# Optimization experiments

Hardware: AMD Instinct MI355X
Metric: run time of the kernel (lower is better)

The kernel has to match this reference:

```python
import jax, jax.numpy as jnp
import numpy as np

N = 50000      # nodes
E = 800000     # edges (before self-loops)
D_IN = 256     # input feature dim
H = 4          # attention heads
C = 32         # per-head channels
HID = H * C    # 128, concat output dim
BN_EPS = 1e-5


def setup_inputs() -> dict:
    key = jax.random.key(0)
    ks = jax.random.split(key, 24)
    inp = {}
    inp["x"] = jax.random.normal(ks[0], (N, D_IN), jnp.float32)
    inp["edge_index"] = jax.random.randint(ks[1], (2, E), 0, N, jnp.int32)
    # layer 1 GATConv params
    inp["W1"] = jax.random.normal(ks[2], (D_IN, HID), jnp.float32) * (2.0 / (D_IN + HID)) ** 0.5
    inp["att_src1"] = jax.random.normal(ks[3], (H, C), jnp.float32) * 0.1
    inp["att_dst1"] = jax.random.normal(ks[4], (H, C), jnp.float32) * 0.1
    inp["bias1"] = jnp.zeros((HID,), jnp.float32)
    # layer 1 BatchNorm (eval mode)
    inp["gamma1"] = 1.0 + 0.1 * jax.random.normal(ks[5], (HID,), jnp.float32)
    inp["beta1"] = 0.1 * jax.random.normal(ks[6], (HID,), jnp.float32)
    inp["mean1"] = 0.1 * jax.random.normal(ks[7], (HID,), jnp.float32)
    inp["var1"] = 0.5 + jax.random.uniform(ks[8], (HID,), jnp.float32)
    # layer 2 GATConv params
    inp["W2"] = jax.random.normal(ks[9], (HID, HID), jnp.float32) * (2.0 / (HID + HID)) ** 0.5
    inp["att_src2"] = jax.random.normal(ks[10], (H, C), jnp.float32) * 0.1
    inp["att_dst2"] = jax.random.normal(ks[11], (H, C), jnp.float32) * 0.1
    inp["bias2"] = jnp.zeros((HID,), jnp.float32)
    # layer 2 BatchNorm (eval mode)
    inp["gamma2"] = 1.0 + 0.1 * jax.random.normal(ks[12], (HID,), jnp.float32)
    inp["beta2"] = 0.1 * jax.random.normal(ks[13], (HID,), jnp.float32)
    inp["mean2"] = 0.1 * jax.random.normal(ks[14], (HID,), jnp.float32)
    inp["var2"] = 0.5 + jax.random.uniform(ks[15], (HID,), jnp.float32)
    return inp


def _gat_layer(x, src, dst, W, att_src, att_dst, bias):
    # x: [N, D]; src/dst: [Etot] with self-loops already appended
    h = (x @ W).reshape(N, H, C)                       # [N, H, C]
    a_s = jnp.einsum("nhc,hc->nh", h, att_src)         # [N, H]
    a_d = jnp.einsum("nhc,hc->nh", h, att_dst)         # [N, H]
    e = jax.nn.leaky_relu(a_s[src] + a_d[dst], 0.2)    # [Etot, H]
    # edge softmax over incoming edges of each destination node
    m = jax.ops.segment_max(e, dst, num_segments=N)    # [N, H]
    ex = jnp.exp(e - m[dst])                           # [Etot, H]
    den = jax.ops.segment_sum(ex, dst, num_segments=N) # [N, H]
    alpha = ex / (den[dst] + 1e-16)                    # [Etot, H]
    out = jax.ops.segment_sum(h[src] * alpha[:, :, None], dst, num_segments=N)
    return out.reshape(N, HID) + bias                  # concat heads + bias


def _bn_eval(x, gamma, beta, mean, var):
    return (x - mean) * (gamma * jax.lax.rsqrt(var + BN_EPS)) + beta


def reference(x, edge_index, W1, att_src1, att_dst1, bias1, gamma1, beta1, mean1, var1,
              W2, att_src2, att_dst2, bias2, gamma2, beta2, mean2, var2):
    loop = jnp.arange(N, dtype=edge_index.dtype)
    src = jnp.concatenate([edge_index[0], loop])  # PyG GATConv adds self-loops
    dst = jnp.concatenate([edge_index[1], loop])
    h = _gat_layer(x, src, dst, W1, att_src1, att_dst1, bias1)
    h = jax.nn.relu(_bn_eval(h, gamma1, beta1, mean1, var1))  # dropout = identity (eval)
    h = _gat_layer(h, src, dst, W2, att_src2, att_dst2, bias2)
    h = jax.nn.relu(_bn_eval(h, gamma2, beta2, mean2, var2))
    return h
```

## Files before the change

kernel.cpp:

```cpp
#include <hip/hip_runtime.h>
#include <math.h>

#define N_NODES 50000
#define EDGES   800000
#define ETOT    (EDGES + N_NODES)
#define HID     128
#define NH      4

typedef __attribute__((ext_vector_type(8))) short short8;
typedef __attribute__((ext_vector_type(4))) float floatx4;

__device__ inline unsigned short f2bf(float f) {
    unsigned int u = __float_as_uint(f);
    u = u + 0x7FFFu + ((u >> 16) & 1u);
    return (unsigned short)(u >> 16);
}

#define NB 391
#define BCAP 2688
#define CHUNK 4096
#define BIN_BLOCKS ((ETOT + CHUNK - 1) / CHUNK)
#define G1A 391

__device__ __forceinline__ void bin_scatter_body(int* histL, int bid,
                                                 const int* __restrict__ ei,
                                                 int* __restrict__ cursor,
                                                 int* __restrict__ binned) {
    int t = threadIdx.x;
    for (int b = t; b < NB; b += 256) histL[b] = 0;
    __syncthreads();
    int base = bid * CHUNK;
#pragma unroll
    for (int j = 0; j < 16; j++) {
        int e = base + j * 256 + t;
        if (e < ETOT) {
            int d = (e < EDGES) ? ei[EDGES + e] : (e - EDGES);
            atomicAdd(&histL[d >> 7], 1);
        }
    }
    __syncthreads();
    for (int b = t; b < NB; b += 256) {
        int c = histL[b];
        histL[b] = c ? (b * BCAP + atomicAdd(&cursor[b], c)) : 0;
    }
    __syncthreads();
#pragma unroll
    for (int j = 0; j < 16; j++) {
        int e = base + j * 256 + t;
        if (e < ETOT) {
            int s, d;
            if (e < EDGES) { s = ei[e]; d = ei[EDGES + e]; }
            else           { s = d = e - EDGES; }
            int bb = d >> 7;
            int pos = atomicAdd(&histL[bb], 1);
            if (pos < (bb + 1) * BCAP)
                binned[pos] = (s << 7) | (d & 127);
        }
    }
}

__device__ __forceinline__ void bin_finalize_body(int* histN, int* excl, int b,
                                                  const int* __restrict__ binned,
                                                  const int* __restrict__ cursor,
                                                  int* __restrict__ starts,
                                                  int* __restrict__ degs,
                                                  int* __restrict__ csr) {
    int t = threadIdx.x;
    int n0 = b << 7;
    int S = b * BCAP;
    int cnt = cursor[b];
    if (cnt > BCAP) cnt = BCAP;
    if (t < 128) histN[t] = 0;
    __syncthreads();
    for (int j = t; j < cnt; j += 256)
        atomicAdd(&histN[binned[S + j] & 127], 1);
    __syncthreads();
    int v = (t < 128) ? histN[t] : 0;
    if (t < 128) excl[t] = v;
    __syncthreads();
    for (int off = 1; off < 128; off <<= 1) {
        int x = 0, add = 0;
        if (t < 128) { x = excl[t]; if (t >= off) add = excl[t - off]; }
        __syncthreads();
        if (t < 128) excl[t] = x + add;
        __syncthreads();
    }
    if (t < 128) {
        int ex = excl[t] - v;
        int n = n0 + t;
        if (n < N_NODES) { starts[n] = S + ex; degs[n] = v; }
        histN[t] = ex;
    }
    __syncthreads();
    for (int j = t; j < cnt; j += 256) {
        int e = binned[S + j];
        int pos = atomicAdd(&histN[e & 127], 1);
        csr[S + pos] = e >> 7;
    }
}

__global__ void wtrans_coef_kernel(const float* __restrict__ W1, const float* __restrict__ W2,
                                   unsigned short* __restrict__ Wt1, unsigned short* __restrict__ Wt2,
                                   const float* __restrict__ b1, const float* __restrict__ g1,
                                   const float* __restrict__ be1, const float* __restrict__ mn1,
                                   const float* __restrict__ vr1,
                                   const float* __restrict__ b2, const float* __restrict__ g2,
                                   const float* __restrict__ be2, const float* __restrict__ mn2,
                                   const float* __restrict__ vr2, float* __restrict__ coef,
                                   int* __restrict__ cursor) {
    int i = blockIdx.x * 256 + threadIdx.x;
    if (i < NB) cursor[i] = 0;
    if (i < 256 * 128) { int k = i >> 7, n = i & 127; Wt1[n * 256 + k] = f2bf(W1[i]); }
    if (i < 128 * 128) { int k = i >> 7, n = i & 127; Wt2[n * 128 + k] = f2bf(W2[i]); }
    if (blockIdx.x == 0) {
        int t = threadIdx.x;
        if (t < 128) {
            float sc = g1[t] * rsqrtf(vr1[t] + 1e-5f);
            coef[t]       = sc;
            coef[128 + t] = be1[t] + (b1[t] - mn1[t]) * sc;
        } else {
            int c = t - 128;
            float sc = g2[c] * rsqrtf(vr2[c] + 1e-5f);
            coef[256 + c] = sc;
            coef[384 + c] = be2[c] + (b2[c] - mn2[c]) * sc;
        }
    }
}

#define GR   64
#define KC   64
#define PADK 88
#define PADH 136

union Smem {
    struct { unsigned short Xs[GR][PADK]; unsigned short Ws[HID][PADK]; } s;
    unsigned short Hs[GR][PADH];
};

template<bool XBF16>
__device__ __forceinline__ void gemm_att_body(Smem& sm, int bid,
                                              const void* __restrict__ Xv,
                                              const unsigned short* __restrict__ Wt,
                                              const float* __restrict__ att_src,
                                              const float* __restrict__ att_dst,
                                              unsigned short* __restrict__ Hout,
                                              float* __restrict__ aS,
                                              float* __restrict__ aD, int K) {
    int t = threadIdx.x, lane = t & 63, w = t >> 6;
    int quad = lane >> 4, nl = lane & 15;
    int rowBase = bid * GR;

    floatx4 acc[8];
    floatx4 zero = {0.f, 0.f, 0.f, 0.f};
#pragma unroll
    for (int b = 0; b < 8; b++) acc[b] = zero;

    const float*          Xf = (const float*)Xv;
    const unsigned short* Xb = (const unsigned short*)Xv;

    for (int k0 = 0; k0 < K; k0 += KC) {
#pragma unroll
        for (int it = 0; it < 2; it++) {
            int s5 = t + it * 256;
            int row = s5 >> 3, kg = s5 & 7;
            int gr = rowBase + row;
            unsigned short tmp[8];
            if (XBF16) {
                uint4 v = make_uint4(0, 0, 0, 0);
                if (gr < N_NODES) v = *(const uint4*)&Xb[(unsigned)(gr * K + k0 + kg * 8)];
                *(uint4*)tmp = v;
            } else {
                float4 v0 = make_float4(0, 0, 0, 0), v1 = v0;
                if (gr < N_NODES) {
                    const float* p = &Xf[(unsigned)(gr * K + k0 + kg * 8)];
                    v0 = *(const float4*)p;
                    v1 = *(const float4*)(p + 4);
                }
                tmp[0] = f2bf(v0.x); tmp[1] = f2bf(v0.y); tmp[2] = f2bf(v0.z); tmp[3] = f2bf(v0.w);
                tmp[4] = f2bf(v1.x); tmp[5] = f2bf(v1.y); tmp[6] = f2bf(v1.z); tmp[7] = f2bf(v1.w);
            }
            *(uint4*)&sm.s.Xs[row][kg * 8] = *(uint4*)tmp;
        }
#pragma unroll
        for (int it = 0; it < 4; it++) {
            int s5 = t + it * 256;
            int n = s5 >> 3, kg = s5 & 7;
            *(uint4*)&sm.s.Ws[n][kg * 8] = *(const uint4*)&Wt[(unsigned)(n * K + k0 + kg * 8)];
        }
        __syncthreads();
#pragma unroll
        for (int ks = 0; ks < 2; ks++) {
            int kb = ks * 32 + quad * 8;
            short8 a0 = *(const short8*)&sm.s.Xs[w * 16 + nl][kb];
#pragma unroll
            for (int ct = 0; ct < 8; ct++) {
                short8 b = *(const short8*)&sm.s.Ws[ct * 16 + nl][kb];
                acc[ct] = __builtin_amdgcn_mfma_f32_16x16x32_bf16(a0, b, acc[ct], 0, 0, 0);
            }
        }
        __syncthreads();
    }

#pragma unroll
    for (int ct = 0; ct < 8; ct++)
#pragma unroll
        for (int r = 0; r < 4; r++)
            sm.Hs[w * 16 + quad * 4 + r][ct * 16 + nl] = f2bf(acc[ct][r]);

    float asv[8], adv[8];
    {
        const float* ap = &att_src[nl * 8];
        const float* dp = &att_dst[nl * 8];
        *(float4*)&asv[0] = *(const float4*)ap;  *(float4*)&asv[4] = *(const float4*)(ap + 4);
        *(float4*)&adv[0] = *(const float4*)dp;  *(float4*)&adv[4] = *(const float4*)(dp + 4);
    }
    int hd = nl >> 2;
#pragma unroll
    for (int it = 0; it < 4; it++) {
        int rl = w * 16 + it * 4 + quad;
        int grow = rowBase + rl;
        uint4 v = *(const uint4*)&sm.Hs[rl][nl * 8];
        float f[8];
        f[0] = __uint_as_float(v.x << 16); f[1] = __uint_as_float(v.x & 0xffff0000u);
        f[2] = __uint_as_float(v.y << 16); f[3] = __uint_as_float(v.y & 0xffff0000u);
        f[4] = __uint_as_float(v.z << 16); f[5] = __uint_as_float(v.z & 0xffff0000u);
        f[6] = __uint_as_float(v.w << 16); f[7] = __uint_as_float(v.w & 0xffff0000u);
        float ds = 0.f, dd = 0.f;
#pragma unroll
        for (int j = 0; j < 8; j++) {
            ds = fmaf(f[j], asv[j], ds);
            dd = fmaf(f[j], adv[j], dd);
        }
        ds += __shfl_xor(ds, 1); ds += __shfl_xor(ds, 2);
        dd += __shfl_xor(dd, 1); dd += __shfl_xor(dd, 2);
        if (grow < N_NODES) {
            *(uint4*)&Hout[(unsigned)(grow * HID + nl * 8)] = v;
            if ((nl & 3) == 0) { aS[grow * 4 + hd] = ds; aD[grow * 4 + hd] = dd; }
        }
    }
}

__global__ __launch_bounds__(256) void fused_scatter_gemm1a(
        const int* __restrict__ ei, int* __restrict__ cursor, int* __restrict__ binned,
        const float* __restrict__ x, const unsigned short* __restrict__ Wt1,
        const float* __restrict__ att_src, const float* __restrict__ att_dst,
        unsigned short* __restrict__ Hout, float* __restrict__ aS, float* __restrict__ aD) {
    __shared__ Smem sm;
    __shared__ int histL[NB];
    if (blockIdx.x < BIN_BLOCKS) {
        bin_scatter_body(histL, blockIdx.x, ei, cursor, binned);
    } else {
        gemm_att_body<false>(sm, blockIdx.x - BIN_BLOCKS, x, Wt1, att_src, att_dst,
                             Hout, aS, aD, 256);
    }
}

__global__ __launch_bounds__(256) void fused_finalize_gemm1b(
        const int* __restrict__ binned, const int* __restrict__ cursor,
        int* __restrict__ starts, int* __restrict__ degs, int* __restrict__ csr,
        const float* __restrict__ x, const unsigned short* __restrict__ Wt1,
        const float* __restrict__ att_src, const float* __restrict__ att_dst,
        unsigned short* __restrict__ Hout, float* __restrict__ aS, float* __restrict__ aD) {
    __shared__ Smem sm;
    __shared__ int histN[128];
    __shared__ int excl[128];
    if (blockIdx.x < NB) {
        bin_finalize_body(histN, excl, blockIdx.x, binned, cursor, starts, degs, csr);
    } else {
        gemm_att_body<false>(sm, blockIdx.x, x, Wt1, att_src, att_dst,
                             Hout, aS, aD, 256);
    }
}

template<bool XBF16>
__global__ __launch_bounds__(256) void gemm_att_kernel(const void* __restrict__ Xv,
                                                       const unsigned short* __restrict__ Wt,
                                                       const float* __restrict__ att_src,
                                                       const float* __restrict__ att_dst,
                                                       unsigned short* __restrict__ Hout,
                                                       float* __restrict__ aS,
                                                       float* __restrict__ aD, int K) {
    __shared__ Smem sm;
    gemm_att_body<XBF16>(sm, blockIdx.x, Xv, Wt, att_src, att_dst, Hout, aS, aD, K);
}

#define ECAP 64

__device__ __forceinline__ void prefetchR(uint4 (&buf)[4], int sregr, const char* hbase,
                                          int sBase, int l16b) {
#pragma unroll
    for (int u = 0; u < 4; u++) {
        int se = __builtin_amdgcn_ds_bpermute(sBase | (u << 2), sregr);
        buf[u] = *(const uint4*)(hbase + (((long)se) << 8) + l16b);
    }
}

__device__ __forceinline__ void consumeR(const uint4 (&buf)[4], float xrr, int aBase,
                                         float (&acc)[8]) {
#pragma unroll
    for (int u = 0; u < 4; u++) {
        float au = __uint_as_float((unsigned)__builtin_amdgcn_ds_bpermute(
                        aBase | (u << 2), (int)__float_as_uint(xrr)));
        uint4 v = buf[u];
        acc[0] = fmaf(__uint_as_float(v.x << 16),         au, acc[0]);
        acc[1] = fmaf(__uint_as_float(v.x & 0xffff0000u), au, acc[1]);
        acc[2] = fmaf(__uint_as_float(v.y << 16),         au, acc[2]);
        acc[3] = fmaf(__uint_as_float(v.y & 0xffff0000u), au, acc[3]);
        acc[4] = fmaf(__uint_as_float(v.z << 16),         au, acc[4]);
        acc[5] = fmaf(__uint_as_float(v.z & 0xffff0000u), au, acc[5]);
        acc[6] = fmaf(__uint_as_float(v.w << 16),         au, acc[6]);
        acc[7] = fmaf(__uint_as_float(v.w & 0xffff0000u), au, acc[7]);
    }
}

template<bool OUTBF16>
__global__ __launch_bounds__(256) void gather_kernel(const unsigned short* __restrict__ hfeat,
                                                     const float* __restrict__ a_s,
                                                     const float* __restrict__ a_d,
                                                     const int* __restrict__ starts,
                                                     const int* __restrict__ degs,
                                                     const int* __restrict__ csr,
                                                     const float* __restrict__ coefA,
                                                     const float* __restrict__ coefB,
                                                     void* __restrict__ outv) {
    int t = threadIdx.x, lane = t & 63, ws = t >> 6;
    int h = lane >> 4, l16 = lane & 15;
    int n = blockIdx.x * 4 + ws;
    int start = starts[n];
    int deg = degs[n];
    float adh = a_d[(unsigned)(n * 4 + h)];
    const char* hbase = (const char*)hfeat;
    int sBase = lane & 48;
    int aBase = ((lane & 12) << 4) | sBase;
    int l16b = l16 << 4;

    int sreg[4];
#pragma unroll
    for (int it = 0; it < 4; it++) {
        int j = l16 + it * 16;
        sreg[it] = (j < deg) ? csr[start + j] : 0;
    }
    float e[4];
#pragma unroll
    for (int it = 0; it < 4; it++) {
        int j = l16 + it * 16;
        e[it] = -1e30f;
        if (j < deg) {
            float as = a_s[(unsigned)(sreg[it] * 4 + h)];
            float v = as + adh;
            e[it] = v > 0.f ? v : 0.2f * v;
        }
    }

    int cap = deg < ECAP ? deg : ECAP;
    uint4 vA[4], vB[4];
    prefetchR(vA, sreg[0], hbase, sBase, l16b);
    if (cap > 16) prefetchR(vB, sreg[1], hbase, sBase, l16b);

    float m = fmaxf(fmaxf(e[0], e[1]), fmaxf(e[2], e[3]));
    for (int j = ECAP + l16; j < deg; j += 16) {
        int s = csr[start + j];
        float as = a_s[(unsigned)(s * 4 + h)];
        float v = as + adh; v = v > 0.f ? v : 0.2f * v;
        m = fmaxf(m, v);
    }
#pragma unroll
    for (int off = 1; off < 16; off <<= 1) m = fmaxf(m, __shfl_xor(m, off));

    float x[4];
    float d = 0.f;
#pragma unroll
    for (int it = 0; it < 4; it++) { x[it] = __expf(e[it] - m); d += x[it]; }
    for (int j = ECAP + l16; j < deg; j += 16) {
        int s = csr[start + j];
        float as = a_s[(unsigned)(s * 4 + h)];
        float v = as + adh; v = v > 0.f ? v : 0.2f * v;
        d += __expf(v - m);
    }
#pragma unroll
    for (int off = 1; off < 16; off <<= 1) d += __shfl_xor(d, off);
    float rd = 1.0f / (d + 1e-16f);
    float xr[4];
#pragma unroll
    for (int it = 0; it < 4; it++) xr[it] = x[it] * rd;

    float acc[8];
#pragma unroll
    for (int j = 0; j < 8; j++) acc[j] = 0.f;
    consumeR(vA, xr[0], aBase, acc);
    if (cap > 16) {
        if (cap > 32) prefetchR(vA, sreg[2], hbase, sBase, l16b);
        consumeR(vB, xr[1], aBase, acc);
        if (cap > 32) {
            if (cap > 48) prefetchR(vB, sreg[3], hbase, sBase, l16b);
            consumeR(vA, xr[2], aBase, acc);
            if (cap > 48) consumeR(vB, xr[3], aBase, acc);
        }
    }
    if (deg > ECAP) {
        int hh = l16 >> 2;
        int gB = (lane & 12) << 4;
        float mB  = __uint_as_float((unsigned)__builtin_amdgcn_ds_bpermute(gB, (int)__float_as_uint(m)));
        float rdB = __uint_as_float((unsigned)__builtin_amdgcn_ds_bpermute(gB, (int)__float_as_uint(rd)));
        float adhB = a_d[(unsigned)(n * 4 + hh)];
        for (int j = ECAP; j < deg; j++) {
            int s = csr[start + j];
            float asv = a_s[(unsigned)(s * 4 + hh)];
            float v2 = asv + adhB; v2 = v2 > 0.f ? v2 : 0.2f * v2;
            float al = __expf(v2 - mB) * rdB;
            uint4 v = *(const uint4*)(hbase + (((long)s) << 8) + l16b);
            acc[0] = fmaf(__uint_as_float(v.x << 16),         al, acc[0]);
            acc[1] = fmaf(__uint_as_float(v.x & 0xffff0000u), al, acc[1]);
            acc[2] = fmaf(__uint_as_float(v.y << 16),         al, acc[2]);
            acc[3] = fmaf(__uint_as_float(v.y & 0xffff0000u), al, acc[3]);
            acc[4] = fmaf(__uint_as_float(v.z << 16),         al, acc[4]);
            acc[5] = fmaf(__uint_as_float(v.z & 0xffff0000u), al, acc[5]);
            acc[6] = fmaf(__uint_as_float(v.w << 16),         al, acc[6]);
            acc[7] = fmaf(__uint_as_float(v.w & 0xffff0000u), al, acc[7]);
        }
    }

#pragma unroll
    for (int j = 0; j < 8; j++) {
        acc[j] += __shfl_xor(acc[j], 16);
        acc[j] += __shfl_xor(acc[j], 32);
    }

    int g = lane >> 4;
    float o0 = acc[0], o1 = acc[1];
    if (g == 1) { o0 = acc[2]; o1 = acc[3]; }
    if (g == 2) { o0 = acc[4]; o1 = acc[5]; }
    if (g == 3) { o0 = acc[6]; o1 = acc[7]; }
    int c = (l16 << 3) + (g << 1);
    float2 cA = *(const float2*)&coefA[c];
    float2 cB = *(const float2*)&coefB[c];
    float r0 = fmaxf(fmaf(o0, cA.x, cB.x), 0.f);
    float r1 = fmaxf(fmaf(o1, cA.y, cB.y), 0.f);
    unsigned oidx = (unsigned)(n * 64 + (l16 << 2) + g);
    if (OUTBF16) {
        unsigned int pk = (unsigned int)f2bf(r0) | ((unsigned int)f2bf(r1) << 16);
        ((unsigned int*)outv)[oidx] = pk;
    } else {
        ((float2*)outv)[oidx] = make_float2(r0, r1);
    }
}

extern "C" void kernel_launch(void* const* d_in, const int* in_sizes, int n_in,
                              void* d_out, int out_size, void* d_ws, size_t ws_size,
                              hipStream_t stream) {
    const float* x    = (const float*)d_in[0];
    const int*   ei   = (const int*)d_in[1];
    const float* W1   = (const float*)d_in[2];
    const float* as1  = (const float*)d_in[3];
    const float* ad1  = (const float*)d_in[4];
    const float* b1   = (const float*)d_in[5];
    const float* g1   = (const float*)d_in[6];
    const float* be1  = (const float*)d_in[7];
    const float* mn1  = (const float*)d_in[8];
    const float* vr1  = (const float*)d_in[9];
    const float* W2   = (const float*)d_in[10];
    const float* as2  = (const float*)d_in[11];
    const float* ad2  = (const float*)d_in[12];
    const float* b2   = (const float*)d_in[13];
    const float* g2   = (const float*)d_in[14];
    const float* be2  = (const float*)d_in[15];
    const float* mn2  = (const float*)d_in[16];
    const float* vr2  = (const float*)d_in[17];
    float* out = (float*)d_out;

    unsigned short* hb  = (unsigned short*)d_ws;
    unsigned short* x2b = hb + (size_t)N_NODES * HID;
    unsigned short* Wt1 = x2b + (size_t)N_NODES * HID;
    unsigned short* Wt2 = Wt1 + 128 * 256;
    float* aS    = (float*)(Wt2 + 128 * 128);
    float* aD    = aS + N_NODES * NH;
    float* coef  = aD + N_NODES * NH;
    int* cursor  = (int*)(coef + 512);
    int* starts  = cursor + NB;
    int* degs    = starts + N_NODES;
    int* binned  = degs + N_NODES;
    int* csr     = binned + NB * BCAP;

    wtrans_coef_kernel<<<128, 256, 0, stream>>>(W1, W2, Wt1, Wt2,
                                                b1, g1, be1, mn1, vr1,
                                                b2, g2, be2, mn2, vr2, coef, cursor);

    int gemmGrid = (N_NODES + GR - 1) / GR;
    int nodeGrid = N_NODES / 4;

    fused_scatter_gemm1a<<<BIN_BLOCKS + G1A, 256, 0, stream>>>(
        ei, cursor, binned, x, Wt1, as1, ad1, hb, aS, aD);
    fused_finalize_gemm1b<<<gemmGrid, 256, 0, stream>>>(
        binned, cursor, starts, degs, csr, x, Wt1, as1, ad1, hb, aS, aD);
    gather_kernel<true><<<nodeGrid, 256, 0, stream>>>(hb, aS, aD, starts, degs, csr,
                                                      coef, coef + 128, (void*)x2b);
    gemm_att_kernel<true><<<gemmGrid, 256, 0, stream>>>(x2b, Wt2, as2, ad2, hb, aS, aD, 128);
    gather_kernel<false><<<nodeGrid, 256, 0, stream>>>(hb, aS, aD, starts, degs, csr,
                                                       coef + 256, coef + 384, (void*)out);
}
```

Measured before the change: 251.2 us.

## Overlap layer-2 GEMM on first half of nodes with layer-1 gather of second half

Splits the layer-1 gather into two halves by node index. The first half runs alone, then a fused kernel runs the layer-2 GEMM for the first node rows alongside the gather for the remaining nodes, and a final GEMM kernel covers the rest of the rows. The goal is to fill the GPU with independent work and cut the serialization between the gather and GEMM stages. This needs separate layer-2 H and attention buffers, which reuse the binned workspace when it is large enough; otherwise the old path runs. It also drops __restrict__ qualifiers and adds one more kernel launch.

```diff
diff --git a/kernel.cpp b/kernel.cpp
--- a/kernel.cpp
+++ b/kernel.cpp
@@ -21,6 +21,8 @@
 #define CHUNK 4096
 #define BIN_BLOCKS ((ETOT + CHUNK - 1) / CHUNK)
 #define G1A 391
+#define NSPLIT 25024
+#define NSPLIT4 6256
 
 __device__ __forceinline__ void bin_scatter_body(int* histL, int bid,
                                                  const int* __restrict__ ei,
@@ -139,13 +141,12 @@
 
 template<bool XBF16>
 __device__ __forceinline__ void gemm_att_body(Smem& sm, int bid,
-                                              const void* __restrict__ Xv,
-                                              const unsigned short* __restrict__ Wt,
-                                              const float* __restrict__ att_src,
-                                              const float* __restrict__ att_dst,
-                                              unsigned short* __restrict__ Hout,
-                                              float* __restrict__ aS,
-                                              float* __restrict__ aD, int K) {
+                                              const void* Xv,
+                                              const unsigned short* Wt,
+                                              const float* att_src,
+                                              const float* att_dst,
+                                              unsigned short* Hout,
+                                              float* aS, float* aD, int K) {
     int t = threadIdx.x, lane = t & 63, w = t >> 6;
     int quad = lane >> 4, nl = lane & 15;
     int rowBase = bid * GR;
@@ -240,50 +241,6 @@
     }
 }
 
-__global__ __launch_bounds__(256) void fused_scatter_gemm1a(
-        const int* __restrict__ ei, int* __restrict__ cursor, int* __restrict__ binned,
-        const float* __restrict__ x, const unsigned short* __restrict__ Wt1,
-        const float* __restrict__ att_src, const float* __restrict__ att_dst,
-        unsigned short* __restrict__ Hout, float* __restrict__ aS, float* __restrict__ aD) {
-    __shared__ Smem sm;
-    __shared__ int histL[NB];
-    if (blockIdx.x < BIN_BLOCKS) {
-        bin_scatter_body(histL, blockIdx.x, ei, cursor, binned);
-    } else {
-        gemm_att_body<false>(sm, blockIdx.x - BIN_BLOCKS, x, Wt1, att_src, att_dst,
-                             Hout, aS, aD, 256);
-    }
-}
-
-__global__ __launch_bounds__(256) void fused_finalize_gemm1b(
-        const int* __restrict__ binned, const int* __restrict__ cursor,
-        int* __restrict__ starts, int* __restrict__ degs, int* __restrict__ csr,
-        const float* __restrict__ x, const unsigned short* __restrict__ Wt1,
-        const float* __restrict__ att_src, const float* __restrict__ att_dst,
-        unsigned short* __restrict__ Hout, float* __restrict__ aS, float* __restrict__ aD) {
-    __shared__ Smem sm;
-    __shared__ int histN[128];
-    __shared__ int excl[128];
-    if (blockIdx.x < NB) {
-        bin_finalize_body(histN, excl, blockIdx.x, binned, cursor, starts, degs, csr);
-    } else {
-        gemm_att_body<false>(sm, blockIdx.x, x, Wt1, att_src, att_dst,
-                             Hout, aS, aD, 256);
-    }
-}
-
-template<bool XBF16>
-__global__ __launch_bounds__(256) void gemm_att_kernel(const void* __restrict__ Xv,
-                                                       const unsigned short* __restrict__ Wt,
-                                                       const float* __restrict__ att_src,
-                                                       const float* __restrict__ att_dst,
-                                                       unsigned short* __restrict__ Hout,
-                                                       float* __restrict__ aS,
-                                                       float* __restrict__ aD, int K) {
-    __shared__ Smem sm;
-    gemm_att_body<XBF16>(sm, blockIdx.x, Xv, Wt, att_src, att_dst, Hout, aS, aD, K);
-}
-
 #define ECAP 64
 
 __device__ __forceinline__ void prefetchR(uint4 (&buf)[4], int sregr, const char* hbase,
@@ -314,18 +271,16 @@
 }
 
 template<bool OUTBF16>
-__global__ __launch_bounds__(256) void gather_kernel(const unsigned short* __restrict__ hfeat,
-                                                     const float* __restrict__ a_s,
-                                                     const float* __restrict__ a_d,
-                                                     const int* __restrict__ starts,
-                                                     const int* __restrict__ degs,
-                                                     const int* __restrict__ csr,
-                                                     const float* __restrict__ coefA,
-                                                     const float* __restrict__ coefB,
-                                                     void* __restrict__ outv) {
+__device__ __forceinline__ void gather_body(int nb,
+                                            const unsigned short* hfeat,
+                                            const float* a_s, const float* a_d,
+                                            const int* starts, const int* degs,
+                                            const int* csr,
+                                            const float* coefA, const float* coefB,
+                                            void* outv) {
     int t = threadIdx.x, lane = t & 63, ws = t >> 6;
     int h = lane >> 4, l16 = lane & 15;
-    int n = blockIdx.x * 4 + ws;
+    int n = nb * 4 + ws;
     int start = starts[n];
     int deg = degs[n];
     float adh = a_d[(unsigned)(n * 4 + h)];
@@ -443,6 +398,77 @@
     } else {
         ((float2*)outv)[oidx] = make_float2(r0, r1);
     }
+}
+
+__global__ __launch_bounds__(256) void fused_scatter_gemm1a(
+        const int* ei, int* cursor, int* binned,
+        const float* x, const unsigned short* Wt1,
+        const float* att_src, const float* att_dst,
+        unsigned short* Hout, float* aS, float* aD) {
+    __shared__ Smem sm;
+    __shared__ int histL[NB];
+    if (blockIdx.x < BIN_BLOCKS) {
+        bin_scatter_body(histL, blockIdx.x, ei, cursor, binned);
+    } else {
+        gemm_att_body<false>(sm, blockIdx.x - BIN_BLOCKS, x, Wt1, att_src, att_dst,
+                             Hout, aS, aD, 256);
+    }
+}
+
+__global__ __launch_bounds__(256) void fused_finalize_gemm1b(
+        const int* binned, const int* cursor,
+        int* starts, int* degs, int* csr,
+        const float* x, const unsigned short* Wt1,
+        const float* att_src, const float* att_dst,
+        unsigned short* Hout, float* aS, float* aD) {
+    __shared__ Smem sm;
+    __shared__ int histN[128];
+    __shared__ int excl[128];
+    if (blockIdx.x < NB) {
+        bin_finalize_body(histN, excl, blockIdx.x, binned, cursor, starts, degs, csr);
+    } else {
+        gemm_att_body<false>(sm, blockIdx.x, x, Wt1, att_src, att_dst,
+                             Hout, aS, aD, 256);
+    }
+}
+
+__global__ __launch_bounds__(256) void fused_gemm2a_gather1b(
+        const unsigned short* x2b, const unsigned short* Wt2,
+        const float* as2, const float* ad2,
+        unsigned short* hbB, float* aS2, float* aD2,
+        const unsigned short* hbA, const float* aS1, const float* aD1,
+        const int* starts, const int* degs, const int* csr,
+        const float* coef1, unsigned short* x2bOut) {
+    __shared__ Smem sm;
+    if (blockIdx.x < G1A) {
+        gemm_att_body<true>(sm, blockIdx.x, x2b, Wt2, as2, ad2, hbB, aS2, aD2, 128);
+    } else {
+        gather_body<true>(NSPLIT4 + (int)blockIdx.x - G1A, hbA, aS1, aD1,
+                          starts, degs, csr, coef1, coef1 + 128, (void*)x2bOut);
+    }
+}
+
+template<bool XBF16>
+__global__ __launch_bounds__(256) void gemm_att_kernel(const void* Xv,
+                                                       const unsigned short* Wt,
+                                                       const float* att_src,
+                                                       const float* att_dst,
+                                                       unsigned short* Hout,
+                                                       float* aS, float* aD,
+                                                       int K, int bidOff) {
+    __shared__ Smem sm;
+    gemm_att_body<XBF16>(sm, blockIdx.x + bidOff, Xv, Wt, att_src, att_dst, Hout, aS, aD, K);
+}
+
+template<bool OUTBF16>
+__global__ __launch_bounds__(256) void gather_kernel(const unsigned short* hfeat,
+                                                     const float* a_s, const float* a_d,
+                                                     const int* starts, const int* degs,
+                                                     const int* csr,
+                                                     const float* coefA, const float* coefB,
+                                                     void* outv, int nbOff) {
+    gather_body<OUTBF16>((int)blockIdx.x + nbOff, hfeat, a_s, a_d, starts, degs, csr,
+                         coefA, coefB, outv);
 }
 
 extern "C" void kernel_launch(void* const* d_in, const int* in_sizes, int n_in,
@@ -468,18 +494,25 @@
     const float* vr2  = (const float*)d_in[17];
     float* out = (float*)d_out;
 
-    unsigned short* hb  = (unsigned short*)d_ws;
-    unsigned short* x2b = hb + (size_t)N_NODES * HID;
+    unsigned short* hbA = (unsigned short*)d_ws;
+    unsigned short* x2b = hbA + (size_t)N_NODES * HID;
     unsigned short* Wt1 = x2b + (size_t)N_NODES * HID;
     unsigned short* Wt2 = Wt1 + 128 * 256;
-    float* aS    = (float*)(Wt2 + 128 * 128);
-    float* aD    = aS + N_NODES * NH;
-    float* coef  = aD + N_NODES * NH;
+    float* aS1   = (float*)(Wt2 + 128 * 128);
+    float* aD1   = aS1 + N_NODES * NH;
+    float* aS2   = aD1 + N_NODES * NH;
+    float* aD2   = aS2 + N_NODES * NH;
+    float* coef  = aD2 + N_NODES * NH;
     int* cursor  = (int*)(coef + 512);
-    int* starts  = cursor + NB;
+    int* starts  = cursor + 512;
     int* degs    = starts + N_NODES;
-    int* binned  = degs + N_NODES;
-    int* csr     = binned + NB * BCAP;
+    int* csr     = degs + N_NODES;
+    int* binned  = csr + NB * BCAP;
+    unsigned short* hbB = (unsigned short*)binned;
+
+    size_t need = (size_t)((char*)binned - (char*)d_ws) + (size_t)N_NODES * HID * 2;
+    bool big = ws_size >= need;
+    if (!big) { hbB = hbA; aS2 = aS1; aD2 = aD1; }
 
     wtrans_coef_kernel<<<128, 256, 0, stream>>>(W1, W2, Wt1, Wt2,
                                                 b1, g1, be1, mn1, vr1,
@@ -489,12 +522,26 @@
     int nodeGrid = N_NODES / 4;
 
     fused_scatter_gemm1a<<<BIN_BLOCKS + G1A, 256, 0, stream>>>(
-        ei, cursor, binned, x, Wt1, as1, ad1, hb, aS, aD);
+        ei, cursor, binned, x, Wt1, as1, ad1, hbA, aS1, aD1);
     fused_finalize_gemm1b<<<gemmGrid, 256, 0, stream>>>(
-        binned, cursor, starts, degs, csr, x, Wt1, as1, ad1, hb, aS, aD);
-    gather_kernel<true><<<nodeGrid, 256, 0, stream>>>(hb, aS, aD, starts, degs, csr,
-                                                      coef, coef + 128, (void*)x2b);
-    gemm_att_kernel<true><<<gemmGrid, 256, 0, stream>>>(x2b, Wt2, as2, ad2, hb, aS, aD, 128);
-    gather_kernel<false><<<nodeGrid, 256, 0, stream>>>(hb, aS, aD, starts, degs, csr,
-                                                       coef + 256, coef + 384, (void*)out);
-}
+        binned, cursor, starts, degs, csr, x, Wt1, as1, ad1, hbA, aS1, aD1);
+
+    if (big) {
+        gather_kernel<true><<<NSPLIT4, 256, 0, stream>>>(hbA, aS1, aD1, starts, degs, csr,
+                                                         coef, coef + 128, (void*)x2b, 0);
+        fused_gemm2a_gather1b<<<G1A + (nodeGrid - NSPLIT4), 256, 0, stream>>>(
+            x2b, Wt2, as2, ad2, hbB, aS2, aD2,
+            hbA, aS1, aD1, starts, degs, csr, coef, x2b);
+        gemm_att_kernel<true><<<gemmGrid - G1A, 256, 0, stream>>>(
+            x2b, Wt2, as2, ad2, hbB, aS2, aD2, 128, G1A);
+        gather_kernel<false><<<nodeGrid, 256, 0, stream>>>(hbB, aS2, aD2, starts, degs, csr,
+                                                           coef + 256, coef + 384, (void*)out, 0);
+    } else {
+        gather_kernel<true><<<nodeGrid, 256, 0, stream>>>(hbA, aS1, aD1, starts, degs, csr,
+                                                          coef, coef + 128, (void*)x2b, 0);
+        gemm_att_kernel<true><<<gemmGrid, 256, 0, stream>>>(x2b, Wt2, as2, ad2, hbA, aS1, aD1,
+                                                            128, 0);
+        gather_kernel<false><<<nodeGrid, 256, 0, stream>>>(hbA, aS1, aD1, starts, degs, csr,
+                                                           coef + 256, coef + 384, (void*)out, 0);
+    }
+}
```

Result: no change. 253.9 us (+1.1%).
